# Kernel optimization log

Measured on AMD Instinct MI355X. Metric: run time of the kernel, lower is better.

## Reference

```python
import jax, jax.numpy as jnp
import numpy as np

K, P, Q, D = 16, 1024, 1024, 64  # heads, value-in dim, out dim, head dim; P'=P, Q'=Q, D'=D
B, N = 2, 2048                   # batch, seq (self-attention: M=N)
TEMPERATURE = jnp.sqrt(jnp.float32(D))

def _xavier(key, shape):
    fan_in, fan_out = shape[-2], shape[-1]
    lim = jnp.sqrt(6.0 / (fan_in + fan_out))
    return jax.random.uniform(key, shape, jnp.float32, -lim, lim)

def setup_inputs() -> dict:
    key = jax.random.key(0)
    k0, k1, k2, k3, k4 = jax.random.split(key, 5)
    return {
        'y_prime': jax.random.normal(k0, (B, N, Q), jnp.float32),
        'mask': jnp.zeros((N, N), jnp.float32),  # log-domain additive mask [M,N]
        'Lam_x': _xavier(k1, (K, P, D)),  # Lambda^(x): [K,P',D']
        'Lam_y': _xavier(k2, (K, Q, D)),  # Lambda^(y): [K,Q',D']
        'Th_x': _xavier(k3, (K, P, D)),   # Theta^(x):  [K,P,D]
        'Th_y': _xavier(k4, (K, Q, D)),   # Theta^(y):  [K,Q,D]
    }

def reference(y_prime, mask, Lam_x, Lam_y, Th_x, Th_y):
    # self-attention: x' = x = y'
    x_p = y_prime
    x = x_p
    # key projection: [B,M,K,D']
    r = jnp.einsum('bmp,kpd->bmkd', x_p, Lam_x)
    # bilinear scores: [K,B,M,N]
    r = jnp.einsum('bmkd,kqd,bnq->kbmn', r, Lam_y, y_prime)
    r = r + mask[None, None, :, :]
    # softmax over M (axis=-2), scaled by sqrt(D')
    A = jax.nn.softmax(r / TEMPERATURE, axis=-2)
    # value aggregation: [B,N,K,D]
    r = jnp.einsum('kbmn,bmp,kpd->bnkd', A, x, Th_x)
    # output projection: [B,N,Q]
    return jnp.einsum('bnkd,kqd->bnq', r, Th_y)
```

## Files before the change

### kernel.cpp

```cpp
#include <hip/hip_runtime.h>
#include <hip/hip_bf16.h>

#define KH 16
#define PD 1024
#define QD 1024
#define DD 64
#define BB 2
#define NN 2048
#define BN 4096
#define ST 72
#define SOFT_C 12.0f
#define LOG2E 1.4426950408889634f
#define SOFT_C2 17.312340490667560f

typedef unsigned short u16;
typedef __attribute__((ext_vector_type(8))) short bf16x8;
typedef __attribute__((ext_vector_type(4))) short bf16x4;
typedef __attribute__((ext_vector_type(4))) float f32x4;

__device__ __forceinline__ float bf2f(u16 u) {
    return __uint_as_float(((unsigned)u) << 16);
}
__device__ __forceinline__ u16 f2bf(float f) {
    unsigned x = __float_as_uint(f);
    x += 0x7FFFu + ((x >> 16) & 1u);
    return (u16)(x >> 16);
}
__device__ __forceinline__ f32x4 mfma_k32(bf16x8 a, bf16x8 b, f32x4 c) {
    return __builtin_amdgcn_mfma_f32_16x16x32_bf16(a, b, c, 0, 0, 0);
}
__device__ __forceinline__ bf16x8 ldfrag(const u16* base, int r0, int kc, int lane) {
    return *reinterpret_cast<const bf16x8*>(base + (r0 + (lane & 15)) * ST + kc +
                                            ((lane >> 4) << 3));
}
__device__ __forceinline__ bf16x4 ldfrag4(const u16* base, int r0, int kc, int lane) {
    return *reinterpret_cast<const bf16x4*>(base + (r0 + (lane & 15)) * ST + kc +
                                            ((lane >> 4) << 2));
}
__device__ __forceinline__ bf16x8 ldfragL(const u16* base, int r0, int kc, int lane) {
    return *reinterpret_cast<const bf16x8*>(base + ((r0 + (lane & 15)) << 6) + kc +
                                            ((lane >> 4) << 3));
}
__device__ __forceinline__ bf16x4 pack4(float a, float b, float c, float d) {
    union { bf16x4 v; __hip_bfloat162 h[2]; } u;
    u.h[0] = __float22bfloat162_rn(make_float2(a, b));
    u.h[1] = __float22bfloat162_rn(make_float2(c, d));
    return u.v;
}
__device__ __forceinline__ void gl_lds16(const u16* g, u16* l) {
    __builtin_amdgcn_global_load_lds(
        (const __attribute__((address_space(1))) void*)g,
        (__attribute__((address_space(3))) void*)l, 16, 0, 0);
}
template <int ROWS>
__device__ __forceinline__ void stage_dma(const u16* __restrict__ src, int ld,
                                          u16* dst, int lane, int w) {
#pragma unroll
    for (int c = 0; c < ROWS / 32; ++c) {
        int rbase = (w * (ROWS / 32) + c) * 8;
        const u16* g = src + (size_t)(rbase + (lane >> 3)) * ld + ((lane & 7) << 3);
        gl_lds16(g, dst + (rbase << 6));
    }
}

__global__ void detect_kernel(const u16* __restrict__ y, int* flag, int* mnz) {
    __shared__ int cnt;
    if (threadIdx.x == 0) cnt = 0;
    __syncthreads();
    int local = 0;
    for (int i = threadIdx.x; i < 8192; i += 256) {
        u16 u = y[i];
        int e = (u >> 7) & 0xFF;
        if (u == 0 || (e >= 96 && e < 160)) local++;
    }
    atomicAdd(&cnt, local);
    __syncthreads();
    if (threadIdx.x == 0) {
        *flag = (cnt > 7372) ? 1 : 0;
        *mnz = 0;
    }
}

__global__ __launch_bounds__(256) void prep_kernel(
    const void* __restrict__ ysrc, const void* __restrict__ msrc,
    const void* __restrict__ s0, const void* __restrict__ s1,
    const void* __restrict__ s2, const void* __restrict__ s3,
    u16* __restrict__ ycan, u16* __restrict__ LamXt, u16* __restrict__ LamYt,
    u16* __restrict__ ThXt, u16* __restrict__ ThYr, u16* __restrict__ maskc,
    const int* __restrict__ flag, int* __restrict__ mnz) {
    int z = blockIdx.z, bx = blockIdx.x, tid = threadIdx.x;
    int isbf = *flag;
    if (z == 0) {
        size_t n4 = (size_t)NN * NN / 8;
        if (!isbf) n4 *= 2;
        const uint4* p = (const uint4*)msrc;
        unsigned acc = 0;
        for (size_t i = (size_t)bx * 256 + tid; i < n4; i += 256 * 256) {
            uint4 v = p[i];
            acc |= v.x | v.y | v.z | v.w;
        }
        if (acc) atomicOr(mnz, 1);
    } else if (z == 1) {
        int n = BN * PD;
        for (int i = (bx * 256 + tid) * 4; i < n; i += 256 * 256 * 4) {
            if (isbf) {
                *reinterpret_cast<uint2*>(ycan + i) =
                    *reinterpret_cast<const uint2*>((const u16*)ysrc + i);
            } else {
                float4 f = *reinterpret_cast<const float4*>((const float*)ysrc + i);
                u16 t[4] = {f2bf(f.x), f2bf(f.y), f2bf(f.z), f2bf(f.w)};
                *reinterpret_cast<uint2*>(ycan + i) = *reinterpret_cast<uint2*>(t);
            }
        }
    } else if (z <= 4) {
        const void* src = (z == 2) ? s0 : (z == 3) ? s1 : s2;
        u16* dst = (z == 2) ? LamXt : (z == 3) ? LamYt : ThXt;
        float scale = (z == 3) ? 0.125f : 1.0f;
        int k = bx >> 4, p0 = (bx & 15) * 64;
        __shared__ float T[64][65];
        const u16* s16 = (const u16*)src + ((size_t)k * PD + p0) * DD;
        const float* s32 = (const float*)src + ((size_t)k * PD + p0) * DD;
#pragma unroll
        for (int it = 0; it < 2; ++it) {
            int chunk = it * 256 + tid;
            int row = chunk >> 3, c8 = (chunk & 7) << 3;
            float f[8];
            if (isbf) {
                uint4 v = *reinterpret_cast<const uint4*>(s16 + row * DD + c8);
                u16 t[8];
                *reinterpret_cast<uint4*>(t) = v;
#pragma unroll
                for (int e = 0; e < 8; ++e) f[e] = bf2f(t[e]);
            } else {
                float4 a = *reinterpret_cast<const float4*>(s32 + row * DD + c8);
                float4 b = *reinterpret_cast<const float4*>(s32 + row * DD + c8 + 4);
                f[0] = a.x; f[1] = a.y; f[2] = a.z; f[3] = a.w;
                f[4] = b.x; f[5] = b.y; f[6] = b.z; f[7] = b.w;
            }
#pragma unroll
            for (int e = 0; e < 8; ++e) T[row][c8 + e] = f[e] * scale;
        }
        __syncthreads();
        u16* drow = dst + (size_t)k * DD * PD + p0;
#pragma unroll
        for (int it = 0; it < 2; ++it) {
            int chunk = it * 256 + tid;
            int d = chunk >> 3, c8 = (chunk & 7) << 3;
            u16 t[8];
#pragma unroll
            for (int e = 0; e < 8; ++e) t[e] = f2bf(T[c8 + e][d]);
            *reinterpret_cast<uint4*>(drow + (size_t)d * PD + c8) =
                *reinterpret_cast<uint4*>(t);
        }
    } else if (z == 5) {
        int k = bx >> 4, q0 = (bx & 15) * 64;
#pragma unroll
        for (int it = 0; it < 2; ++it) {
            int chunk = it * 256 + tid;
            int row = chunk >> 3, c8 = (chunk & 7) << 3;
            size_t si = ((size_t)k * QD + q0 + row) * DD + c8;
            u16 t[8];
            if (isbf) {
                *reinterpret_cast<uint4*>(t) =
                    *reinterpret_cast<const uint4*>((const u16*)s3 + si);
            } else {
                float4 a = *reinterpret_cast<const float4*>((const float*)s3 + si);
                float4 b = *reinterpret_cast<const float4*>((const float*)s3 + si + 4);
                t[0] = f2bf(a.x); t[1] = f2bf(a.y); t[2] = f2bf(a.z); t[3] = f2bf(a.w);
                t[4] = f2bf(b.x); t[5] = f2bf(b.y); t[6] = f2bf(b.z); t[7] = f2bf(b.w);
            }
            *reinterpret_cast<uint4*>(ThYr + (size_t)(q0 + row) * (KH * DD) +
                                      k * DD + c8) = *reinterpret_cast<uint4*>(t);
        }
    } else {
        size_t n8 = (size_t)NN * NN / 8;
        for (size_t c = (size_t)bx * 256 + tid; c < n8; c += 256 * 256) {
            size_t i = c * 8;
            float f[8];
            if (isbf) {
                uint4 v = *reinterpret_cast<const uint4*>((const u16*)msrc + i);
                u16 t[8];
                *reinterpret_cast<uint4*>(t) = v;
#pragma unroll
                for (int e = 0; e < 8; ++e) f[e] = bf2f(t[e]);
            } else {
                float4 a = *reinterpret_cast<const float4*>((const float*)msrc + i);
                float4 b = *reinterpret_cast<const float4*>((const float*)msrc + i + 4);
                f[0] = a.x; f[1] = a.y; f[2] = a.z; f[3] = a.w;
                f[4] = b.x; f[5] = b.y; f[6] = b.z; f[7] = b.w;
            }
            u16 t[8];
#pragma unroll
            for (int e = 0; e < 8; ++e) t[e] = f2bf(f[e] * 0.125f);
            *reinterpret_cast<uint4*>(maskc + i) = *reinterpret_cast<uint4*>(t);
        }
    }
}

__global__ __launch_bounds__(256, 3) void proj_gemm(
    const u16* __restrict__ A,
    const u16* __restrict__ Bm,
    u16* __restrict__ Xk, u16* __restrict__ Yk, u16* __restrict__ Vtg) {
    int tid = threadIdx.x, lane = tid & 63, w = tid >> 6;
    int mhalf = w & 1, nhalf = w >> 1;
    int m0 = blockIdx.x * 128, n0 = blockIdx.y * 128;
    __shared__ u16 As[128 * 64];
    __shared__ u16 Bs[128 * 64];
    f32x4 acc[4][4] = {};

    for (int kk = 0; kk < PD; kk += 64) {
        __syncthreads();
        stage_dma<128>(A + (size_t)m0 * PD + kk, PD, As, lane, w);
        stage_dma<128>(Bm + (size_t)n0 * PD + kk, PD, Bs, lane, w);
        __syncthreads();
#pragma unroll
        for (int kc = 0; kc < 64; kc += 32) {
            bf16x8 af[4], bf[4];
#pragma unroll
            for (int i = 0; i < 4; ++i) af[i] = ldfragL(As, mhalf * 64 + i * 16, kc, lane);
#pragma unroll
            for (int j = 0; j < 4; ++j) bf[j] = ldfragL(Bs, nhalf * 64 + j * 16, kc, lane);
#pragma unroll
            for (int i = 0; i < 4; ++i)
#pragma unroll
                for (int j = 0; j < 4; ++j) acc[i][j] = mfma_k32(af[i], bf[j], acc[i][j]);
        }
    }
    int s = n0 >> 10;
    int quad = lane >> 4, col = lane & 15;
    u16* stg = nhalf ? Bs : As;
    __syncthreads();
    if (s == 2) {
#pragma unroll
        for (int i = 0; i < 4; ++i)
#pragma unroll
            for (int j = 0; j < 4; ++j)
                *reinterpret_cast<bf16x4*>(stg + (j * 16 + col) * 128 + mhalf * 64 +
                                           i * 16 + quad * 4) =
                    pack4(acc[i][j][0], acc[i][j][1], acc[i][j][2], acc[i][j][3]);
    } else {
#pragma unroll
        for (int i = 0; i < 4; ++i)
#pragma unroll
            for (int j = 0; j < 4; ++j)
#pragma unroll
                for (int reg = 0; reg < 4; ++reg)
                    stg[(mhalf * 64 + i * 16 + quad * 4 + reg) * 64 + j * 16 + col] =
                        f2bf(acc[i][j][reg]);
    }
    __syncthreads();
#pragma unroll
    for (int h = 0; h < 2; ++h) {
        int kh = ((n0 + h * 64) >> 6) & 15;
        const u16* src = h ? Bs : As;
        if (s == 2) {
            u16* vb = Vtg + (size_t)kh * DD * BN + m0;
#pragma unroll
            for (int it = 0; it < 4; ++it) {
                int chunk = it * 256 + tid;
                int d = chunk >> 4, off = (chunk & 15) * 8;
                *reinterpret_cast<uint4*>(vb + (size_t)d * BN + off) =
                    *reinterpret_cast<const uint4*>(src + d * 128 + off);
            }
        } else {
            u16* ob = (s == 0 ? Xk : Yk) + (size_t)kh * BN * DD + (size_t)m0 * DD;
#pragma unroll
            for (int it = 0; it < 4; ++it) {
                int chunk = it * 256 + tid;
                *reinterpret_cast<uint4*>(ob + chunk * 8) =
                    *reinterpret_cast<const uint4*>(src + chunk * 8);
            }
        }
    }
}

__global__ __launch_bounds__(512, 4) void attn_kernel(
    const u16* __restrict__ Xk,
    const u16* __restrict__ Yk,
    const u16* __restrict__ Vtg,
    const u16* __restrict__ maskc,
    const int* __restrict__ mnz,
    u16* __restrict__ O) {
    int tid = threadIdx.x, lane = tid & 63, w = tid >> 6;
    int quad = lane >> 4, col = lane & 15;
    int par = w >> 2;
    int wq = w & 3;
    int q0 = blockIdx.x * 128, k = blockIdx.y, b = blockIdx.z;
    const u16* Qp = Yk + ((size_t)k * BN + b * NN + q0) * DD;
    const u16* Kp = Xk + ((size_t)k * BN + b * NN) * DD;
    const u16* Vp = Vtg + (size_t)k * DD * BN + b * NN;
    __shared__ u16 smem[2 * 3 * 64 * ST];
    u16* Kb0 = smem;
    u16* Vb0 = smem + 3 * 64 * ST;
    int mz = *mnz;

    bf16x8 qf[2][2];
#pragma unroll
    for (int qg = 0; qg < 2; ++qg) {
        const u16* qrow = Qp + (size_t)(wq * 32 + qg * 16 + col) * DD + (quad << 3);
        qf[qg][0] = *reinterpret_cast<const bf16x8*>(qrow);
        qf[qg][1] = *reinterpret_cast<const bf16x8*>(qrow + 32);
    }

    int srow = tid >> 3, scol = (tid & 7) << 3;
    const u16* kgp = Kp + (size_t)srow * DD + scol;
    const u16* vgp = Vp + (size_t)srow * BN + scol;
    int soff = srow * ST + scol;

    uint4 kr = *reinterpret_cast<const uint4*>(kgp);
    uint4 vr = *reinterpret_cast<const uint4*>(vgp);
    *reinterpret_cast<uint4*>(Kb0 + soff) = kr;
    *reinterpret_cast<uint4*>(Vb0 + soff) = vr;
    kr = *reinterpret_cast<const uint4*>(kgp + (size_t)64 * DD);
    vr = *reinterpret_cast<const uint4*>(vgp + 64);
    __syncthreads();

    float lp[2] = {0.0f, 0.0f};
    f32x4 oacc[4][2] = {};

    for (int t = 0; t < 32; ++t) {
        int cur = t % 3;
        if (t < 31) {
            int nxt = (t + 1) % 3;
            *reinterpret_cast<uint4*>(Kb0 + nxt * (64 * ST) + soff) = kr;
            *reinterpret_cast<uint4*>(Vb0 + nxt * (64 * ST) + soff) = vr;
            if (t < 30) {
                kr = *reinterpret_cast<const uint4*>(kgp + (size_t)(t + 2) * 64 * DD);
                vr = *reinterpret_cast<const uint4*>(vgp + (t + 2) * 64);
            }
            __syncthreads();
        }
        if ((t & 1) != par) continue;
        const u16* Ks = Kb0 + cur * (64 * ST);
        const u16* Vt = Vb0 + cur * (64 * ST);
        int m0 = t * 64;

        bf16x4 pb4[4][2];
#pragma unroll
        for (int kg = 0; kg < 4; ++kg) {
            bf16x8 a0 = ldfrag(Ks, kg * 16, 0, lane);
            bf16x8 a1 = ldfrag(Ks, kg * 16, 32, lane);
#pragma unroll
            for (int qg = 0; qg < 2; ++qg) {
                f32x4 s = {};
                s = mfma_k32(a0, qf[qg][0], s);
                s = mfma_k32(a1, qf[qg][1], s);
                if (mz) {
#pragma unroll
                    for (int reg = 0; reg < 4; ++reg)
                        s[reg] += bf2f(
                            maskc[(size_t)(m0 + kg * 16 + quad * 4 + reg) * NN +
                                  q0 + wq * 32 + qg * 16 + col]);
                }
                float p0 = exp2f(fmaf(s[0], LOG2E, -SOFT_C2));
                float p1 = exp2f(fmaf(s[1], LOG2E, -SOFT_C2));
                float p2 = exp2f(fmaf(s[2], LOG2E, -SOFT_C2));
                float p3 = exp2f(fmaf(s[3], LOG2E, -SOFT_C2));
                lp[qg] += (p0 + p1) + (p2 + p3);
                pb4[kg][qg] = pack4(p0, p1, p2, p3);
            }
        }
#pragma unroll
        for (int half = 0; half < 2; ++half) {
            bf16x8 pb8[2];
#pragma unroll
            for (int qg = 0; qg < 2; ++qg)
                pb8[qg] = __builtin_shufflevector(pb4[half * 2][qg],
                                                  pb4[half * 2 + 1][qg],
                                                  0, 1, 2, 3, 4, 5, 6, 7);
#pragma unroll
            for (int dg = 0; dg < 4; ++dg) {
                bf16x4 v0 = ldfrag4(Vt, dg * 16, half * 32, lane);
                bf16x4 v1 = ldfrag4(Vt, dg * 16, half * 32 + 16, lane);
                bf16x8 av = __builtin_shufflevector(v0, v1, 0, 1, 2, 3, 4, 5, 6, 7);
#pragma unroll
                for (int qg = 0; qg < 2; ++qg)
                    oacc[dg][qg] = mfma_k32(av, pb8[qg], oacc[dg][qg]);
            }
        }
    }

    __syncthreads();
    float* red = (float*)smem;
    const int RS = 66;
    if (par == 1) {
#pragma unroll
        for (int qg = 0; qg < 2; ++qg) {
            float l2 = lp[qg];
            l2 += __shfl_xor(l2, 16);
            l2 += __shfl_xor(l2, 32);
            int q = wq * 32 + qg * 16 + col;
            if (quad == 0) red[q * RS + 64] = l2;
#pragma unroll
            for (int dg = 0; dg < 4; ++dg) {
                *reinterpret_cast<float2*>(red + q * RS + dg * 16 + quad * 4) =
                    make_float2(oacc[dg][qg][0], oacc[dg][qg][1]);
                *reinterpret_cast<float2*>(red + q * RS + dg * 16 + quad * 4 + 2) =
                    make_float2(oacc[dg][qg][2], oacc[dg][qg][3]);
            }
        }
    }
    __syncthreads();
    u16* Ost = smem + 2 * 3 * 64 * ST - 128 * ST;
    if (par == 0) {
#pragma unroll
        for (int qg = 0; qg < 2; ++qg) {
            int q = wq * 32 + qg * 16 + col;
            float l2 = lp[qg];
            l2 += __shfl_xor(l2, 16);
            l2 += __shfl_xor(l2, 32);
            l2 += red[q * RS + 64];
            float inv = 1.0f / l2;
#pragma unroll
            for (int dg = 0; dg < 4; ++dg) {
                float2 r0 = *reinterpret_cast<const float2*>(red + q * RS + dg * 16 +
                                                             quad * 4);
                float2 r1 = *reinterpret_cast<const float2*>(red + q * RS + dg * 16 +
                                                             quad * 4 + 2);
                *reinterpret_cast<bf16x4*>(Ost + q * ST + dg * 16 + quad * 4) =
                    pack4((oacc[dg][qg][0] + r0.x) * inv,
                          (oacc[dg][qg][1] + r0.y) * inv,
                          (oacc[dg][qg][2] + r1.x) * inv,
                          (oacc[dg][qg][3] + r1.y) * inv);
            }
        }
    }
    __syncthreads();
#pragma unroll
    for (int it = 0; it < 2; ++it) {
        int chunk = it * 512 + tid;
        int row = chunk >> 3, c8 = (chunk & 7) << 3;
        *reinterpret_cast<uint4*>(O + (size_t)(b * NN + q0 + row) * (KH * DD) +
                                  k * DD + c8) =
            *reinterpret_cast<const uint4*>(Ost + row * ST + c8);
    }
}

__global__ __launch_bounds__(256, 3) void out_gemm(
    const u16* __restrict__ A,
    const u16* __restrict__ Bm,
    const int* __restrict__ flag,
    void* __restrict__ outv) {
    int tid = threadIdx.x, lane = tid & 63, w = tid >> 6;
    int mhalf = w & 1, nhalf = w >> 1;
    int m0 = blockIdx.x * 128, n0 = blockIdx.y * 128;
    __shared__ u16 S[2][128 * 64];
    u16* As = S[0];
    u16* Bs = S[1];
    f32x4 acc[4][4] = {};

    for (int kk = 0; kk < KH * DD; kk += 64) {
        __syncthreads();
        stage_dma<128>(A + (size_t)m0 * (KH * DD) + kk, KH * DD, As, lane, w);
        stage_dma<128>(Bm + (size_t)n0 * (KH * DD) + kk, KH * DD, Bs, lane, w);
        __syncthreads();
#pragma unroll
        for (int kc = 0; kc < 64; kc += 32) {
            bf16x8 af[4], bf[4];
#pragma unroll
            for (int i = 0; i < 4; ++i) af[i] = ldfragL(As, mhalf * 64 + i * 16, kc, lane);
#pragma unroll
            for (int j = 0; j < 4; ++j) bf[j] = ldfragL(Bs, nhalf * 64 + j * 16, kc, lane);
#pragma unroll
            for (int i = 0; i < 4; ++i)
#pragma unroll
                for (int j = 0; j < 4; ++j) acc[i][j] = mfma_k32(af[i], bf[j], acc[i][j]);
        }
    }
    int isbf = *flag;
    int quad = lane >> 4, col = lane & 15;
    if (isbf) {
#pragma unroll
        for (int i = 0; i < 4; ++i)
#pragma unroll
            for (int j = 0; j < 4; ++j)
#pragma unroll
                for (int reg = 0; reg < 4; ++reg) {
                    size_t row = m0 + mhalf * 64 + i * 16 + quad * 4 + reg;
                    int c = n0 + nhalf * 64 + j * 16 + col;
                    ((u16*)outv)[row * QD + c] = f2bf(acc[i][j][reg]);
                }
    } else {
        float* Sf = (float*)&S[0][0];
#pragma unroll
        for (int h = 0; h < 2; ++h) {
            __syncthreads();
            if (mhalf == h) {
#pragma unroll
                for (int i = 0; i < 4; ++i)
#pragma unroll
                    for (int j = 0; j < 4; ++j)
#pragma unroll
                        for (int reg = 0; reg < 4; ++reg)
                            Sf[(i * 16 + quad * 4 + reg) * 128 + nhalf * 64 +
                               j * 16 + col] = acc[i][j][reg];
            }
            __syncthreads();
            float* orow = (float*)outv + (size_t)(m0 + h * 64) * QD + n0;
#pragma unroll
            for (int it = 0; it < 8; ++it) {
                int chunk = it * 256 + tid;
                int row = chunk >> 5, c4 = (chunk & 31) * 4;
                *reinterpret_cast<float4*>(orow + (size_t)row * QD + c4) =
                    *reinterpret_cast<const float4*>(Sf + row * 128 + c4);
            }
        }
    }
}

extern "C" void kernel_launch(void* const* d_in, const int* in_sizes, int n_in,
                              void* d_out, int out_size, void* d_ws, size_t ws_size,
                              hipStream_t stream) {
    char* wsb = (char*)d_ws;
    int* flag = (int*)wsb;
    int* mnz = (int*)(wsb + 16);
    u16* ycan = (u16*)(wsb + 64);
    const size_t NYP = (size_t)BN * PD;
    const size_t NW = (size_t)KH * PD * DD;
    const size_t OSZ = (size_t)BN * KH * DD;
    u16* Wcat = ycan + NYP;
    u16* ThYr = Wcat + 3 * NW;
    u16* Xk = ThYr + NW;
    u16* Yk = Xk + OSZ;
    u16* Vtg = Yk + OSZ;
    u16* maskc = Vtg + OSZ;
    u16* Ob = ycan;

    detect_kernel<<<1, 256, 0, stream>>>((const u16*)d_in[0], flag, mnz);
    prep_kernel<<<dim3(256, 1, 7), 256, 0, stream>>>(
        d_in[0], d_in[1], d_in[2], d_in[3], d_in[4], d_in[5], ycan, Wcat,
        Wcat + NW, Wcat + 2 * NW, ThYr, maskc, flag, mnz);
    proj_gemm<<<dim3(BN / 128, 3072 / 128), 256, 0, stream>>>(ycan, Wcat, Xk, Yk, Vtg);
    attn_kernel<<<dim3(NN / 128, KH, BB), 512, 0, stream>>>(Xk, Yk, Vtg, maskc,
                                                            mnz, Ob);
    out_gemm<<<dim3(BN / 128, QD / 128), 256, 0, stream>>>(Ob, ThYr, flag, d_out);
}
```

Baseline: 237.3 us.

## Load attention K/V fragments directly from global into registers, drop LDS staging

The attention kernel stops staging K and V tiles in shared memory with a triple buffer and barriers. Each wave now loads its MFMA fragments straight from global (L2-cached) memory, prefetching the next K tile into registers. The block shrinks to 4 waves with no split-M reduction, and block IDs are remapped so blocks sharing a head land on the same XCD. To match the new V fragment layout, the proj_gemm V-transpose store is permuted. This removes LDS traffic and barriers, but it adds redundant global loads across waves and higher register pressure.

```diff
diff --git a/kernel.cpp b/kernel.cpp
--- a/kernel.cpp
+++ b/kernel.cpp
@@ -28,14 +28,6 @@
 }
 __device__ __forceinline__ f32x4 mfma_k32(bf16x8 a, bf16x8 b, f32x4 c) {
     return __builtin_amdgcn_mfma_f32_16x16x32_bf16(a, b, c, 0, 0, 0);
-}
-__device__ __forceinline__ bf16x8 ldfrag(const u16* base, int r0, int kc, int lane) {
-    return *reinterpret_cast<const bf16x8*>(base + (r0 + (lane & 15)) * ST + kc +
-                                            ((lane >> 4) << 3));
-}
-__device__ __forceinline__ bf16x4 ldfrag4(const u16* base, int r0, int kc, int lane) {
-    return *reinterpret_cast<const bf16x4*>(base + (r0 + (lane & 15)) * ST + kc +
-                                            ((lane >> 4) << 2));
 }
 __device__ __forceinline__ bf16x8 ldfragL(const u16* base, int r0, int kc, int lane) {
     return *reinterpret_cast<const bf16x8*>(base + ((r0 + (lane & 15)) << 6) + kc +
@@ -235,8 +227,9 @@
         for (int i = 0; i < 4; ++i)
 #pragma unroll
             for (int j = 0; j < 4; ++j)
-                *reinterpret_cast<bf16x4*>(stg + (j * 16 + col) * 128 + mhalf * 64 +
-                                           i * 16 + quad * 4) =
+                *reinterpret_cast<bf16x4*>(stg + (j * 16 + col) * 128 +
+                                           (mhalf * 2 + (i >> 1)) * 32 +
+                                           quad * 8 + (i & 1) * 4) =
                     pack4(acc[i][j][0], acc[i][j][1], acc[i][j][2], acc[i][j][3]);
     } else {
 #pragma unroll
@@ -274,24 +267,22 @@
     }
 }
 
-__global__ __launch_bounds__(512, 4) void attn_kernel(
+__global__ __launch_bounds__(256, 2) void attn_kernel(
     const u16* __restrict__ Xk,
     const u16* __restrict__ Yk,
     const u16* __restrict__ Vtg,
     const u16* __restrict__ maskc,
     const int* __restrict__ mnz,
     u16* __restrict__ O) {
-    int tid = threadIdx.x, lane = tid & 63, w = tid >> 6;
+    int tid = threadIdx.x, lane = tid & 63, wq = tid >> 6;
     int quad = lane >> 4, col = lane & 15;
-    int par = w >> 2;
-    int wq = w & 3;
-    int q0 = blockIdx.x * 128, k = blockIdx.y, b = blockIdx.z;
+    int H = blockIdx.x;
+    int L = (H & 7) * 64 + (H >> 3);
+    int q0 = (L & 15) * 128, k = (L >> 4) & 15, b = L >> 8;
     const u16* Qp = Yk + ((size_t)k * BN + b * NN + q0) * DD;
     const u16* Kp = Xk + ((size_t)k * BN + b * NN) * DD;
     const u16* Vp = Vtg + (size_t)k * DD * BN + b * NN;
-    __shared__ u16 smem[2 * 3 * 64 * ST];
-    u16* Kb0 = smem;
-    u16* Vb0 = smem + 3 * 64 * ST;
+    __shared__ u16 Ost[128 * ST];
     int mz = *mnz;
 
     bf16x8 qf[2][2];
@@ -301,50 +292,48 @@
         qf[qg][0] = *reinterpret_cast<const bf16x8*>(qrow);
         qf[qg][1] = *reinterpret_cast<const bf16x8*>(qrow + 32);
     }
-
-    int srow = tid >> 3, scol = (tid & 7) << 3;
-    const u16* kgp = Kp + (size_t)srow * DD + scol;
-    const u16* vgp = Vp + (size_t)srow * BN + scol;
-    int soff = srow * ST + scol;
-
-    uint4 kr = *reinterpret_cast<const uint4*>(kgp);
-    uint4 vr = *reinterpret_cast<const uint4*>(vgp);
-    *reinterpret_cast<uint4*>(Kb0 + soff) = kr;
-    *reinterpret_cast<uint4*>(Vb0 + soff) = vr;
-    kr = *reinterpret_cast<const uint4*>(kgp + (size_t)64 * DD);
-    vr = *reinterpret_cast<const uint4*>(vgp + 64);
-    __syncthreads();
+    const u16* kb = Kp + (size_t)(lane & 15) * DD + (quad << 3);
+    const u16* vb = Vp + (size_t)(lane & 15) * BN + (quad << 3);
 
     float lp[2] = {0.0f, 0.0f};
     f32x4 oacc[4][2] = {};
 
+    bf16x8 kf[4][2];
+#pragma unroll
+    for (int kg = 0; kg < 4; ++kg) {
+        const u16* kp = kb + (size_t)(kg * 16) * DD;
+        kf[kg][0] = *reinterpret_cast<const bf16x8*>(kp);
+        kf[kg][1] = *reinterpret_cast<const bf16x8*>(kp + 32);
+    }
+
     for (int t = 0; t < 32; ++t) {
-        int cur = t % 3;
+        const u16* vt = vb + t * 64;
+        bf16x8 av[2][4];
+#pragma unroll
+        for (int half = 0; half < 2; ++half)
+#pragma unroll
+            for (int dg = 0; dg < 4; ++dg)
+                av[half][dg] = *reinterpret_cast<const bf16x8*>(
+                    vt + (size_t)(dg * 16) * BN + half * 32);
+        bf16x8 kn[4][2];
         if (t < 31) {
-            int nxt = (t + 1) % 3;
-            *reinterpret_cast<uint4*>(Kb0 + nxt * (64 * ST) + soff) = kr;
-            *reinterpret_cast<uint4*>(Vb0 + nxt * (64 * ST) + soff) = vr;
-            if (t < 30) {
-                kr = *reinterpret_cast<const uint4*>(kgp + (size_t)(t + 2) * 64 * DD);
-                vr = *reinterpret_cast<const uint4*>(vgp + (t + 2) * 64);
-            }
-            __syncthreads();
-        }
-        if ((t & 1) != par) continue;
-        const u16* Ks = Kb0 + cur * (64 * ST);
-        const u16* Vt = Vb0 + cur * (64 * ST);
+            const u16* knb = kb + (size_t)(t + 1) * 64 * DD;
+#pragma unroll
+            for (int kg = 0; kg < 4; ++kg) {
+                const u16* kp = knb + (size_t)(kg * 16) * DD;
+                kn[kg][0] = *reinterpret_cast<const bf16x8*>(kp);
+                kn[kg][1] = *reinterpret_cast<const bf16x8*>(kp + 32);
+            }
+        }
         int m0 = t * 64;
-
         bf16x4 pb4[4][2];
 #pragma unroll
         for (int kg = 0; kg < 4; ++kg) {
-            bf16x8 a0 = ldfrag(Ks, kg * 16, 0, lane);
-            bf16x8 a1 = ldfrag(Ks, kg * 16, 32, lane);
 #pragma unroll
             for (int qg = 0; qg < 2; ++qg) {
                 f32x4 s = {};
-                s = mfma_k32(a0, qf[qg][0], s);
-                s = mfma_k32(a1, qf[qg][1], s);
+                s = mfma_k32(kf[kg][0], qf[qg][0], s);
+                s = mfma_k32(kf[kg][1], qf[qg][1], s);
                 if (mz) {
 #pragma unroll
                     for (int reg = 0; reg < 4; ++reg)
@@ -369,66 +358,35 @@
                                                   pb4[half * 2 + 1][qg],
                                                   0, 1, 2, 3, 4, 5, 6, 7);
 #pragma unroll
-            for (int dg = 0; dg < 4; ++dg) {
-                bf16x4 v0 = ldfrag4(Vt, dg * 16, half * 32, lane);
-                bf16x4 v1 = ldfrag4(Vt, dg * 16, half * 32 + 16, lane);
-                bf16x8 av = __builtin_shufflevector(v0, v1, 0, 1, 2, 3, 4, 5, 6, 7);
+            for (int dg = 0; dg < 4; ++dg)
 #pragma unroll
                 for (int qg = 0; qg < 2; ++qg)
-                    oacc[dg][qg] = mfma_k32(av, pb8[qg], oacc[dg][qg]);
-            }
-        }
-    }
-
+                    oacc[dg][qg] = mfma_k32(av[half][dg], pb8[qg], oacc[dg][qg]);
+        }
+#pragma unroll
+        for (int kg = 0; kg < 4; ++kg) {
+            kf[kg][0] = kn[kg][0];
+            kf[kg][1] = kn[kg][1];
+        }
+    }
+
+#pragma unroll
+    for (int qg = 0; qg < 2; ++qg) {
+        float l2 = lp[qg];
+        l2 += __shfl_xor(l2, 16);
+        l2 += __shfl_xor(l2, 32);
+        float inv = 1.0f / l2;
+        int q = wq * 32 + qg * 16 + col;
+#pragma unroll
+        for (int dg = 0; dg < 4; ++dg)
+            *reinterpret_cast<bf16x4*>(Ost + q * ST + dg * 16 + quad * 4) =
+                pack4(oacc[dg][qg][0] * inv, oacc[dg][qg][1] * inv,
+                      oacc[dg][qg][2] * inv, oacc[dg][qg][3] * inv);
+    }
     __syncthreads();
-    float* red = (float*)smem;
-    const int RS = 66;
-    if (par == 1) {
-#pragma unroll
-        for (int qg = 0; qg < 2; ++qg) {
-            float l2 = lp[qg];
-            l2 += __shfl_xor(l2, 16);
-            l2 += __shfl_xor(l2, 32);
-            int q = wq * 32 + qg * 16 + col;
-            if (quad == 0) red[q * RS + 64] = l2;
-#pragma unroll
-            for (int dg = 0; dg < 4; ++dg) {
-                *reinterpret_cast<float2*>(red + q * RS + dg * 16 + quad * 4) =
-                    make_float2(oacc[dg][qg][0], oacc[dg][qg][1]);
-                *reinterpret_cast<float2*>(red + q * RS + dg * 16 + quad * 4 + 2) =
-                    make_float2(oacc[dg][qg][2], oacc[dg][qg][3]);
-            }
-        }
-    }
-    __syncthreads();
-    u16* Ost = smem + 2 * 3 * 64 * ST - 128 * ST;
-    if (par == 0) {
-#pragma unroll
-        for (int qg = 0; qg < 2; ++qg) {
-            int q = wq * 32 + qg * 16 + col;
-            float l2 = lp[qg];
-            l2 += __shfl_xor(l2, 16);
-            l2 += __shfl_xor(l2, 32);
-            l2 += red[q * RS + 64];
-            float inv = 1.0f / l2;
-#pragma unroll
-            for (int dg = 0; dg < 4; ++dg) {
-                float2 r0 = *reinterpret_cast<const float2*>(red + q * RS + dg * 16 +
-                                                             quad * 4);
-                float2 r1 = *reinterpret_cast<const float2*>(red + q * RS + dg * 16 +
-                                                             quad * 4 + 2);
-                *reinterpret_cast<bf16x4*>(Ost + q * ST + dg * 16 + quad * 4) =
-                    pack4((oacc[dg][qg][0] + r0.x) * inv,
-                          (oacc[dg][qg][1] + r0.y) * inv,
-                          (oacc[dg][qg][2] + r1.x) * inv,
-                          (oacc[dg][qg][3] + r1.y) * inv);
-            }
-        }
-    }
-    __syncthreads();
-#pragma unroll
-    for (int it = 0; it < 2; ++it) {
-        int chunk = it * 512 + tid;
+#pragma unroll
+    for (int it = 0; it < 4; ++it) {
+        int chunk = it * 256 + tid;
         int row = chunk >> 3, c8 = (chunk & 7) << 3;
         *reinterpret_cast<uint4*>(O + (size_t)(b * NN + q0 + row) * (KH * DD) +
                                   k * DD + c8) =
@@ -531,7 +489,6 @@
         d_in[0], d_in[1], d_in[2], d_in[3], d_in[4], d_in[5], ycan, Wcat,
         Wcat + NW, Wcat + 2 * NW, ThYr, maskc, flag, mnz);
     proj_gemm<<<dim3(BN / 128, 3072 / 128), 256, 0, stream>>>(ycan, Wcat, Xk, Yk, Vtg);
-    attn_kernel<<<dim3(NN / 128, KH, BB), 512, 0, stream>>>(Xk, Yk, Vtg, maskc,
-                                                            mnz, Ob);
+    attn_kernel<<<512, 256, 0, stream>>>(Xk, Yk, Vtg, maskc, mnz, Ob);
     out_gemm<<<dim3(BN / 128, QD / 128), 256, 0, stream>>>(Ob, ThYr, flag, d_out);
 }
```

After: 288.1 us. 21.4% more time.
